# Performance work log

Hardware: AMD Instinct MI355X
Metric: run time of the kernel (lower is better)

The kernel has to match this reference:

```python
import jax, jax.numpy as jnp
import numpy as np

D_MODEL = 384
N_HEAD = 6
HEAD_SIZE = 64
T_LEN = 256
BATCH = 128


def layernorm(x, g, b, eps=1e-5):
    mu = jnp.mean(x, axis=-1, keepdims=True)
    var = jnp.mean(jnp.square(x - mu), axis=-1, keepdims=True)
    return (x - mu) * jax.lax.rsqrt(var + eps) * g + b


def setup_inputs() -> dict:
    key = jax.random.key(0)
    ks = jax.random.split(key, 16)
    s = 0.02
    return {
        "x": jax.random.normal(ks[0], (BATCH, T_LEN, D_MODEL), jnp.float32),
        "Wq": jax.random.normal(ks[1], (N_HEAD, D_MODEL, HEAD_SIZE), jnp.float32) * s,
        "Wk": jax.random.normal(ks[2], (N_HEAD, D_MODEL, HEAD_SIZE), jnp.float32) * s,
        "Wv": jax.random.normal(ks[3], (N_HEAD, D_MODEL, HEAD_SIZE), jnp.float32) * s,
        "Wp": jax.random.normal(ks[4], (N_HEAD * HEAD_SIZE, D_MODEL), jnp.float32) * s,
        "bp": jnp.zeros((D_MODEL,), jnp.float32),
        "W1": jax.random.normal(ks[5], (D_MODEL, 4 * D_MODEL), jnp.float32) * s,
        "b1": jnp.zeros((4 * D_MODEL,), jnp.float32),
        "W2": jax.random.normal(ks[6], (4 * D_MODEL, D_MODEL), jnp.float32) * s,
        "b2": jnp.zeros((D_MODEL,), jnp.float32),
        "g1": jnp.ones((D_MODEL,), jnp.float32),
        "be1": jnp.zeros((D_MODEL,), jnp.float32),
        "g2": jnp.ones((D_MODEL,), jnp.float32),
        "be2": jnp.zeros((D_MODEL,), jnp.float32),
    }


def reference(x, Wq, Wk, Wv, Wp, bp, W1, b1, W2, b2, g1, be1, g2, be2):
    B, T, C = x.shape
    # --- pre-LN causal multi-head attention ---
    h = layernorm(x, g1, be1)
    q = jnp.einsum('btd,hde->bhte', h, Wq)  # [B,H,T,E]
    k = jnp.einsum('btd,hde->bhte', h, Wk)
    v = jnp.einsum('btd,hde->bhte', h, Wv)
    scores = jnp.einsum('bhte,bhse->bhts', q, k) / jnp.sqrt(jnp.float32(HEAD_SIZE))
    causal = jnp.tril(jnp.ones((T, T), bool))
    scores = jnp.where(causal, scores, jnp.float32(-jnp.inf))
    wei = jax.nn.softmax(scores, axis=-1)  # dropout = identity (eval)
    out = jnp.einsum('bhts,bhse->bhte', wei, v)
    out = out.transpose(0, 2, 1, 3).reshape(B, T, N_HEAD * HEAD_SIZE)  # head-concat
    x = x + out @ Wp + bp
    # --- pre-LN FFN ---
    h2 = layernorm(x, g2, be2)
    ff = jax.nn.relu(h2 @ W1 + b1) @ W2 + b2
    return x + ff
```

## Files before the change

kernel.cpp:

```cpp
#include <hip/hip_runtime.h>
#include <hip/hip_bf16.h>

#define D_MODEL 384
#define N_HEAD  6
#define HEAD    64
#define T_LEN   256
#define BATCH   128
#define MROWS   (BATCH * T_LEN)
#define FF      1536

typedef __bf16 bf16x8 __attribute__((ext_vector_type(8)));
typedef float  f32x4  __attribute__((ext_vector_type(4)));
typedef unsigned short us8 __attribute__((ext_vector_type(8)));
typedef unsigned short us4 __attribute__((ext_vector_type(4)));
using bf16 = __hip_bfloat16;

__device__ inline f32x4 mfma16(bf16x8 a, bf16x8 b, f32x4 c) {
    return __builtin_amdgcn_mfma_f32_16x16x32_bf16(a, b, c, 0, 0, 0);
}

#define GLOAD_LDS16(g, l) __builtin_amdgcn_global_load_lds( \
    (const __attribute__((address_space(1))) unsigned int*)(g), \
    (__attribute__((address_space(3))) unsigned int*)(l), 16, 0, 0)

__global__ __launch_bounds__(256) void prep_w(
    const float* __restrict__ Wq, const float* __restrict__ Wk, const float* __restrict__ Wv,
    const float* __restrict__ Wp, const float* __restrict__ W1, const float* __restrict__ W2,
    bf16* __restrict__ Wqkv_t, bf16* __restrict__ Wp_t,
    bf16* __restrict__ W1_t,   bf16* __restrict__ W2_t)
{
    int i = blockIdx.x * 256 + threadIdx.x;
    if (i < 1152 * 384) {
        int cc = i / 384, d = i - cc * 384;
        const float* src = cc < 384 ? Wq : (cc < 768 ? Wk : Wv);
        int c = cc < 384 ? cc : (cc < 768 ? cc - 384 : cc - 768);
        int h = c >> 6, e = c & 63;
        Wqkv_t[i] = __float2bfloat16(src[(h * 384 + d) * 64 + e]);
    }
    if (i < 384 * 384) {
        int o = i / 384, d = i - o * 384;
        Wp_t[i] = __float2bfloat16(Wp[d * 384 + o]);
    }
    if (i < 1536 * 384) {
        int o = i / 384, d = i - o * 384;
        W1_t[i] = __float2bfloat16(W1[d * 1536 + o]);
        int o2 = i / 1536, d2 = i - o2 * 1536;
        W2_t[i] = __float2bfloat16(W2[d2 * 384 + o2]);
    }
}

__global__ __launch_bounds__(256) void ln_k(
    const float* __restrict__ xin, const float* __restrict__ gg,
    const float* __restrict__ bb, bf16* __restrict__ outb)
{
    int wid  = blockIdx.x * 4 + (threadIdx.x >> 6);
    int lane = threadIdx.x & 63;
    const float* xr = xin + (size_t)wid * 384;
    float v[6]; float s = 0.f;
#pragma unroll
    for (int i = 0; i < 6; ++i) { v[i] = xr[lane + i * 64]; s += v[i]; }
#pragma unroll
    for (int mk = 1; mk < 64; mk <<= 1) s += __shfl_xor(s, mk);
    float mu = s * (1.f / 384.f);
    float vs = 0.f;
#pragma unroll
    for (int i = 0; i < 6; ++i) { float d = v[i] - mu; vs += d * d; }
#pragma unroll
    for (int mk = 1; mk < 64; mk <<= 1) vs += __shfl_xor(vs, mk);
    float rs = rsqrtf(vs * (1.f / 384.f) + 1e-5f);
    bf16* orow = outb + (size_t)wid * 384;
#pragma unroll
    for (int i = 0; i < 6; ++i) {
        int c = lane + i * 64;
        orow[c] = __float2bfloat16((v[i] - mu) * rs * gg[c] + bb[c]);
    }
}

__global__ __launch_bounds__(256) void tr_v(
    const bf16* __restrict__ qkv, bf16* __restrict__ vT)
{
    __shared__ bf16 L[256][68];
    int bh = blockIdx.x;
    int b = bh / N_HEAD, h = bh - b * N_HEAD;
    int tid = threadIdx.x;
    const bf16* src = qkv + (size_t)(b * T_LEN + tid) * 1152 + 768 + h * 64;
#pragma unroll
    for (int c = 0; c < 8; ++c)
        *(us8*)&L[tid][c * 8] = *(const us8*)&src[c * 8];
    __syncthreads();
    bf16* dst = vT + (size_t)bh * HEAD * T_LEN;
#pragma unroll
    for (int i = 0; i < 8; ++i) {
        int idx = tid + i * 256;
        int e = idx >> 5, tc = (idx & 31) * 8;
        bf16x8 pk;
#pragma unroll
        for (int j = 0; j < 8; ++j) pk[j] = *(__bf16*)&L[tc + j][e];
        *(bf16x8*)&dst[(size_t)e * T_LEN + tc] = pk;
    }
}

enum { EPI_QKV = 0, EPI_PROJ = 1, EPI_FFN1 = 2, EPI_FFN2 = 3 };

template<int EPI, int K, int NTN>
__global__ __launch_bounds__(256, 2) void gemm8(
    const bf16* __restrict__ A, const bf16* __restrict__ Bt,
    const float* __restrict__ bias, const float* __restrict__ resid,
    float* __restrict__ outf, bf16* __restrict__ outq, bf16* __restrict__ outb)
{
    extern __shared__ char smem[];
    bf16* Albase = (bf16*)smem;
    bf16* Blbase = (bf16*)(smem + 32768);
    constexpr int NT = K / 64;
    constexpr int nwg = (MROWS / 128) * NTN;
    int bid = blockIdx.x;
    int wg = (bid & 7) * (nwg >> 3) + (bid >> 3);
    int mt = wg / NTN, nt = wg - mt * NTN;
    int m0 = mt * 128, n0 = nt * 128;
    int tid = threadIdx.x, lane = tid & 63, w = tid >> 6;
    int r = lane & 15, g = lane >> 4;
    int lr8 = lane >> 3, l7 = lane & 7;
    int csw = (l7 ^ lr8) << 3;
    int wm = (w >> 1) * 64, wn = (w & 1) * 64;
    int sb = g ^ l7;

    const bf16* Ag = A  + (size_t)(m0 + w * 32 + lr8) * K + csw;
    const bf16* Bg = Bt + (size_t)(n0 + w * 32 + lr8) * K + csw;
    const int L0 = w * 2048;

#define STAGE(tt, bb) do { \
    const bf16* a_ = Ag + (tt) * 64; \
    const bf16* b_ = Bg + (tt) * 64; \
    bf16* al_ = Albase + (bb) * 8192 + L0; \
    bf16* bl_ = Blbase + (bb) * 8192 + L0; \
    _Pragma("unroll") for (int q_ = 0; q_ < 4; ++q_) \
        GLOAD_LDS16(a_ + (size_t)q_ * 8 * K, al_ + q_ * 512); \
    _Pragma("unroll") for (int q_ = 0; q_ < 4; ++q_) \
        GLOAD_LDS16(b_ + (size_t)q_ * 8 * K, bl_ + q_ * 512); \
} while (0)

    f32x4 acc[4][4];
#pragma unroll
    for (int i = 0; i < 4; ++i)
#pragma unroll
        for (int j = 0; j < 4; ++j) acc[i][j] = (f32x4){0.f, 0.f, 0.f, 0.f};

    STAGE(0, 0);
    STAGE(1, 1);

#define ITER(tt, VMS, DOSTAGE) do { \
    int bb_ = (tt) & 1; \
    asm volatile("s_waitcnt vmcnt(" VMS ")" ::: "memory"); \
    __builtin_amdgcn_s_barrier(); \
    __builtin_amdgcn_sched_barrier(0); \
    const bf16* Ar_ = Albase + bb_ * 8192; \
    const bf16* Br_ = Blbase + bb_ * 8192; \
    _Pragma("unroll") for (int kk = 0; kk < 2; ++kk) { \
        int so_ = (sb ^ (kk * 4)) << 3; \
        bf16x8 af[4], bfv[4]; \
        _Pragma("unroll") for (int mi = 0; mi < 4; ++mi) \
            af[mi] = *(const bf16x8*)&Ar_[(wm + mi * 16 + r) * 64 + so_]; \
        _Pragma("unroll") for (int ni = 0; ni < 4; ++ni) \
            bfv[ni] = *(const bf16x8*)&Br_[(wn + ni * 16 + r) * 64 + so_]; \
        asm volatile("s_waitcnt lgkmcnt(0)" ::: "memory"); \
        __builtin_amdgcn_sched_barrier(0); \
        __builtin_amdgcn_s_setprio(1); \
        _Pragma("unroll") for (int mi = 0; mi < 4; ++mi) \
            _Pragma("unroll") for (int ni = 0; ni < 4; ++ni) \
                acc[mi][ni] = mfma16(bfv[ni], af[mi], acc[mi][ni]); \
        __builtin_amdgcn_s_setprio(0); \
    } \
    __builtin_amdgcn_s_barrier(); \
    if (DOSTAGE) STAGE((tt) + 2, bb_); \
} while (0)

#pragma unroll 1
    for (int t = 0; t < NT - 2; ++t) ITER(t, "8", true);
    ITER(NT - 2, "8", false);
    ITER(NT - 1, "0", false);
#undef ITER
#undef STAGE

#pragma unroll
    for (int mi = 0; mi < 4; ++mi) {
        size_t m = m0 + wm + mi * 16 + r;
#pragma unroll
        for (int ni = 0; ni < 4; ++ni) {
            int nb = n0 + wn + ni * 16 + (g << 2);
            f32x4 a = acc[mi][ni];
            if constexpr (EPI == EPI_QKV) {
                us4 u;
#pragma unroll
                for (int j = 0; j < 4; ++j) {
                    __bf16 hb = (__bf16)a[j];
                    u[j] = __builtin_bit_cast(unsigned short, hb);
                }
                *(us4*)&outq[m * 1152 + nb] = u;
            } else if constexpr (EPI == EPI_FFN1) {
                f32x4 b4 = *(const f32x4*)&bias[nb];
                us4 u;
#pragma unroll
                for (int j = 0; j < 4; ++j) {
                    float z = a[j] + b4[j]; z = z > 0.f ? z : 0.f;
                    __bf16 hb = (__bf16)z;
                    u[j] = __builtin_bit_cast(unsigned short, hb);
                }
                *(us4*)&outb[m * FF + nb] = u;
            } else {
                f32x4 b4 = *(const f32x4*)&bias[nb];
                f32x4 rv = *(const f32x4*)&resid[m * 384 + nb];
                f32x4 o;
#pragma unroll
                for (int j = 0; j < 4; ++j) o[j] = rv[j] + a[j] + b4[j];
                *(f32x4*)&outf[m * 384 + nb] = o;
            }
        }
    }
}

__global__ __launch_bounds__(256) void attn_k(
    const bf16* __restrict__ qkv, const bf16* __restrict__ vT,
    bf16* __restrict__ att)
{
    __shared__ bf16 Ksm[2][64][64];
    __shared__ bf16 Vsm[2][64][64];
    __shared__ bf16 Psm[4][16][72];
    int bid = blockIdx.x;
    int wg = (bid & 7) * 384 + (bid >> 3);
    int qt = wg & 3, bh = wg >> 2;
    int b = bh / N_HEAD, h = bh - b * N_HEAD;
    int q0 = qt * 64;
    int tid = threadIdx.x, lane = tid & 63, w = tid >> 6;
    int r = lane & 15, g = lane >> 4, ko = g << 3;
    int lr = lane >> 3, l7 = lane & 7;
    int csw = (l7 ^ lr) << 3;
    int r7 = r & 7;

    const bf16* qbase = qkv + (size_t)b * T_LEN * 1152 + h * 64;
    const bf16* kbase = qbase + 384;
    const bf16* vbase = vT + (size_t)bh * HEAD * T_LEN;

#define STAGEA(st, bb) do { \
    int s0_ = (st) * 64; \
    _Pragma("unroll") for (int s_ = 0; s_ < 2; ++s_) { \
        int row0_ = w * 16 + s_ * 8; \
        GLOAD_LDS16(kbase + (size_t)(s0_ + row0_ + lr) * 1152 + csw, &Ksm[bb][row0_][0]); \
        GLOAD_LDS16(vbase + (size_t)(row0_ + lr) * T_LEN + s0_ + csw, &Vsm[bb][row0_][0]); \
    } \
} while (0)

    STAGEA(0, 0);

    bf16x8 qf[2];
    qf[0] = *(const bf16x8*)&qbase[(size_t)(q0 + w * 16 + r) * 1152 + ko];
    qf[1] = *(const bf16x8*)&qbase[(size_t)(q0 + w * 16 + r) * 1152 + ko + 32];

    f32x4 o[4];
#pragma unroll
    for (int i = 0; i < 4; ++i) o[i] = (f32x4){0.f, 0.f, 0.f, 0.f};
    float mrow[4], lrow[4];
#pragma unroll
    for (int j = 0; j < 4; ++j) { mrow[j] = -3.0e38f; lrow[j] = 0.f; }

    for (int st = 0; st <= qt; ++st) {
        int buf = st & 1;
        __syncthreads();
        if (st < qt) STAGEA(st + 1, buf ^ 1);

        f32x4 s[4];
#pragma unroll
        for (int i = 0; i < 4; ++i) s[i] = (f32x4){0.f, 0.f, 0.f, 0.f};
#pragma unroll
        for (int kk = 0; kk < 2; ++kk) {
#pragma unroll
            for (int ni = 0; ni < 4; ++ni) {
                bf16x8 kf = *(const bf16x8*)&Ksm[buf][ni * 16 + r][((4 * kk + g) ^ r7) << 3];
                s[ni] = mfma16(qf[kk], kf, s[ni]);
            }
        }
        int qrow = q0 + w * 16 + (g << 2);
        int s0 = st * 64;
        float tmax[4], fsc[4], tsum[4];
#pragma unroll
        for (int j = 0; j < 4; ++j) {
            float mx = -3.0e38f;
#pragma unroll
            for (int ni = 0; ni < 4; ++ni) {
                int col = s0 + ni * 16 + r;
                float sv = (col <= qrow + j) ? s[ni][j] * 0.125f : -3.0e38f;
                s[ni][j] = sv;
                mx = fmaxf(mx, sv);
            }
            tmax[j] = mx;
        }
#pragma unroll
        for (int mk = 1; mk < 16; mk <<= 1)
#pragma unroll
            for (int j = 0; j < 4; ++j) tmax[j] = fmaxf(tmax[j], __shfl_xor(tmax[j], mk));
#pragma unroll
        for (int j = 0; j < 4; ++j) {
            float mnew = fmaxf(mrow[j], tmax[j]);
            fsc[j] = __expf(mrow[j] - mnew);
            mrow[j] = mnew;
            float ss = 0.f;
#pragma unroll
            for (int ni = 0; ni < 4; ++ni) {
                float p = __expf(s[ni][j] - mnew);
                s[ni][j] = p; ss += p;
            }
            tsum[j] = ss;
        }
#pragma unroll
        for (int mk = 1; mk < 16; mk <<= 1)
#pragma unroll
            for (int j = 0; j < 4; ++j) tsum[j] += __shfl_xor(tsum[j], mk);
#pragma unroll
        for (int j = 0; j < 4; ++j) lrow[j] = lrow[j] * fsc[j] + tsum[j];
#pragma unroll
        for (int ni = 0; ni < 4; ++ni)
#pragma unroll
            for (int j = 0; j < 4; ++j) o[ni][j] *= fsc[j];
#pragma unroll
        for (int ni = 0; ni < 4; ++ni)
#pragma unroll
            for (int j = 0; j < 4; ++j)
                Psm[w][(g << 2) + j][ni * 16 + r] = __float2bfloat16(s[ni][j]);
#pragma unroll
        for (int kk = 0; kk < 2; ++kk) {
            bf16x8 pf = *(const bf16x8*)&Psm[w][r][kk * 32 + ko];
#pragma unroll
            for (int ni = 0; ni < 4; ++ni) {
                bf16x8 vf = *(const bf16x8*)&Vsm[buf][ni * 16 + r][((4 * kk + g) ^ r7) << 3];
                o[ni] = mfma16(pf, vf, o[ni]);
            }
        }
    }
#undef STAGEA

#pragma unroll
    for (int ni = 0; ni < 4; ++ni)
#pragma unroll
        for (int j = 0; j < 4; ++j) {
            int t = q0 + w * 16 + (g << 2) + j;
            int e = h * HEAD + ni * 16 + r;
            att[((size_t)b * T_LEN + t) * D_MODEL + e] = __float2bfloat16(o[ni][j] / lrow[j]);
        }
}

#define GEMM_SMEM 65536

extern "C" void kernel_launch(void* const* d_in, const int* in_sizes, int n_in,
                              void* d_out, int out_size, void* d_ws, size_t ws_size,
                              hipStream_t stream)
{
    const float* x   = (const float*)d_in[0];
    const float* Wq  = (const float*)d_in[1];
    const float* Wk  = (const float*)d_in[2];
    const float* Wv  = (const float*)d_in[3];
    const float* Wp  = (const float*)d_in[4];
    const float* bp  = (const float*)d_in[5];
    const float* W1  = (const float*)d_in[6];
    const float* b1  = (const float*)d_in[7];
    const float* W2  = (const float*)d_in[8];
    const float* b2  = (const float*)d_in[9];
    const float* g1  = (const float*)d_in[10];
    const float* be1 = (const float*)d_in[11];
    const float* g2  = (const float*)d_in[12];
    const float* be2 = (const float*)d_in[13];
    float* out = (float*)d_out;

    char* ws = (char*)d_ws;
    size_t off = 0;
    auto alloc = [&](size_t bytes) { void* p = ws + off; off += (bytes + 255) & ~(size_t)255; return p; };
    bf16* Wqkv_t = (bf16*)alloc((size_t)1152 * 384 * 2);
    bf16* Wp_t   = (bf16*)alloc((size_t)384 * 384 * 2);
    bf16* W1_t   = (bf16*)alloc((size_t)1536 * 384 * 2);
    bf16* W2_t   = (bf16*)alloc((size_t)384 * 1536 * 2);
    bf16* h      = (bf16*)alloc((size_t)MROWS * 384 * 2);
    bf16* qkv    = (bf16*)alloc((size_t)MROWS * 1152 * 2);
    bf16* attb   = (bf16*)alloc((size_t)MROWS * 384 * 2);
    float* x1    = (float*)alloc((size_t)MROWS * 384 * 4);
    bf16* vTb    = h;
    bf16* ff1    = qkv;

    hipFuncSetAttribute(reinterpret_cast<const void*>(&gemm8<EPI_QKV, 384, 9>),
                        hipFuncAttributeMaxDynamicSharedMemorySize, GEMM_SMEM);
    hipFuncSetAttribute(reinterpret_cast<const void*>(&gemm8<EPI_PROJ, 384, 3>),
                        hipFuncAttributeMaxDynamicSharedMemorySize, GEMM_SMEM);
    hipFuncSetAttribute(reinterpret_cast<const void*>(&gemm8<EPI_FFN1, 384, 12>),
                        hipFuncAttributeMaxDynamicSharedMemorySize, GEMM_SMEM);
    hipFuncSetAttribute(reinterpret_cast<const void*>(&gemm8<EPI_FFN2, 1536, 3>),
                        hipFuncAttributeMaxDynamicSharedMemorySize, GEMM_SMEM);

    prep_w<<<2304, 256, 0, stream>>>(Wq, Wk, Wv, Wp, W1, W2, Wqkv_t, Wp_t, W1_t, W2_t);
    ln_k<<<MROWS / 4, 256, 0, stream>>>(x, g1, be1, h);
    gemm8<EPI_QKV, 384, 9><<<2304, 256, GEMM_SMEM, stream>>>(
        h, Wqkv_t, nullptr, nullptr, nullptr, qkv, nullptr);
    tr_v<<<BATCH * N_HEAD, 256, 0, stream>>>(qkv, vTb);
    attn_k<<<BATCH * N_HEAD * 4, 256, 0, stream>>>(qkv, vTb, attb);
    gemm8<EPI_PROJ, 384, 3><<<768, 256, GEMM_SMEM, stream>>>(
        attb, Wp_t, bp, x, x1, nullptr, nullptr);
    ln_k<<<MROWS / 4, 256, 0, stream>>>(x1, g2, be2, h);
    gemm8<EPI_FFN1, 384, 12><<<3072, 256, GEMM_SMEM, stream>>>(
        h, W1_t, b1, nullptr, nullptr, nullptr, ff1);
    gemm8<EPI_FFN2, 1536, 3><<<768, 256, GEMM_SMEM, stream>>>(
        ff1, W2_t, b2, x1, out, nullptr, nullptr);
}
```

Before: 302.1 us.

## Drop GEMM double buffering for single-buffered static LDS at higher occupancy

Replaces the hand-scheduled double-buffered GEMM mainloop (explicit vmcnt waits, sched barriers, setprio) with a simple single-buffered loop using static 32KB shared memory and two __syncthreads per K tile. Launch bounds rise from 2 to 4 blocks per CU, relying on extra waves to hide global-to-LDS latency instead of software prefetch. The exchange is lost intra-block overlap between loads and MFMA, plus extra barriers, for potentially more concurrent blocks, with register pressure possibly constrained by the tighter bound.

```diff
diff --git a/kernel.cpp b/kernel.cpp
--- a/kernel.cpp
+++ b/kernel.cpp
@@ -103,14 +103,13 @@
 enum { EPI_QKV = 0, EPI_PROJ = 1, EPI_FFN1 = 2, EPI_FFN2 = 3 };
 
 template<int EPI, int K, int NTN>
-__global__ __launch_bounds__(256, 2) void gemm8(
+__global__ __launch_bounds__(256, 4) void gemm8(
     const bf16* __restrict__ A, const bf16* __restrict__ Bt,
     const float* __restrict__ bias, const float* __restrict__ resid,
     float* __restrict__ outf, bf16* __restrict__ outq, bf16* __restrict__ outb)
 {
-    extern __shared__ char smem[];
-    bf16* Albase = (bf16*)smem;
-    bf16* Blbase = (bf16*)(smem + 32768);
+    __shared__ bf16 Asm[128][64];
+    __shared__ bf16 Bsm[128][64];
     constexpr int NT = K / 64;
     constexpr int nwg = (MROWS / 128) * NTN;
     int bid = blockIdx.x;
@@ -126,18 +125,8 @@
 
     const bf16* Ag = A  + (size_t)(m0 + w * 32 + lr8) * K + csw;
     const bf16* Bg = Bt + (size_t)(n0 + w * 32 + lr8) * K + csw;
-    const int L0 = w * 2048;
-
-#define STAGE(tt, bb) do { \
-    const bf16* a_ = Ag + (tt) * 64; \
-    const bf16* b_ = Bg + (tt) * 64; \
-    bf16* al_ = Albase + (bb) * 8192 + L0; \
-    bf16* bl_ = Blbase + (bb) * 8192 + L0; \
-    _Pragma("unroll") for (int q_ = 0; q_ < 4; ++q_) \
-        GLOAD_LDS16(a_ + (size_t)q_ * 8 * K, al_ + q_ * 512); \
-    _Pragma("unroll") for (int q_ = 0; q_ < 4; ++q_) \
-        GLOAD_LDS16(b_ + (size_t)q_ * 8 * K, bl_ + q_ * 512); \
-} while (0)
+    bf16* Al = &Asm[w * 32][0];
+    bf16* Bl = &Bsm[w * 32][0];
 
     f32x4 acc[4][4];
 #pragma unroll
@@ -145,41 +134,34 @@
 #pragma unroll
         for (int j = 0; j < 4; ++j) acc[i][j] = (f32x4){0.f, 0.f, 0.f, 0.f};
 
-    STAGE(0, 0);
-    STAGE(1, 1);
-
-#define ITER(tt, VMS, DOSTAGE) do { \
-    int bb_ = (tt) & 1; \
-    asm volatile("s_waitcnt vmcnt(" VMS ")" ::: "memory"); \
-    __builtin_amdgcn_s_barrier(); \
-    __builtin_amdgcn_sched_barrier(0); \
-    const bf16* Ar_ = Albase + bb_ * 8192; \
-    const bf16* Br_ = Blbase + bb_ * 8192; \
-    _Pragma("unroll") for (int kk = 0; kk < 2; ++kk) { \
-        int so_ = (sb ^ (kk * 4)) << 3; \
-        bf16x8 af[4], bfv[4]; \
-        _Pragma("unroll") for (int mi = 0; mi < 4; ++mi) \
-            af[mi] = *(const bf16x8*)&Ar_[(wm + mi * 16 + r) * 64 + so_]; \
-        _Pragma("unroll") for (int ni = 0; ni < 4; ++ni) \
-            bfv[ni] = *(const bf16x8*)&Br_[(wn + ni * 16 + r) * 64 + so_]; \
-        asm volatile("s_waitcnt lgkmcnt(0)" ::: "memory"); \
-        __builtin_amdgcn_sched_barrier(0); \
-        __builtin_amdgcn_s_setprio(1); \
-        _Pragma("unroll") for (int mi = 0; mi < 4; ++mi) \
-            _Pragma("unroll") for (int ni = 0; ni < 4; ++ni) \
-                acc[mi][ni] = mfma16(bfv[ni], af[mi], acc[mi][ni]); \
-        __builtin_amdgcn_s_setprio(0); \
-    } \
-    __builtin_amdgcn_s_barrier(); \
-    if (DOSTAGE) STAGE((tt) + 2, bb_); \
-} while (0)
-
 #pragma unroll 1
-    for (int t = 0; t < NT - 2; ++t) ITER(t, "8", true);
-    ITER(NT - 2, "8", false);
-    ITER(NT - 1, "0", false);
-#undef ITER
-#undef STAGE
+    for (int t = 0; t < NT; ++t) {
+        const bf16* a_ = Ag + t * 64;
+        const bf16* b_ = Bg + t * 64;
+#pragma unroll
+        for (int q = 0; q < 4; ++q) {
+            GLOAD_LDS16(a_ + (size_t)q * 8 * K, Al + q * 512);
+            GLOAD_LDS16(b_ + (size_t)q * 8 * K, Bl + q * 512);
+        }
+        __syncthreads();
+#pragma unroll
+        for (int kk = 0; kk < 2; ++kk) {
+            int so = (sb ^ (kk * 4)) << 3;
+            bf16x8 af[4], bfv[4];
+#pragma unroll
+            for (int mi = 0; mi < 4; ++mi)
+                af[mi] = *(const bf16x8*)&Asm[wm + mi * 16 + r][so];
+#pragma unroll
+            for (int ni = 0; ni < 4; ++ni)
+                bfv[ni] = *(const bf16x8*)&Bsm[wn + ni * 16 + r][so];
+#pragma unroll
+            for (int mi = 0; mi < 4; ++mi)
+#pragma unroll
+                for (int ni = 0; ni < 4; ++ni)
+                    acc[mi][ni] = mfma16(bfv[ni], af[mi], acc[mi][ni]);
+        }
+        __syncthreads();
+    }
 
 #pragma unroll
     for (int mi = 0; mi < 4; ++mi) {
@@ -346,8 +328,6 @@
             att[((size_t)b * T_LEN + t) * D_MODEL + e] = __float2bfloat16(o[ni][j] / lrow[j]);
         }
 }
-
-#define GEMM_SMEM 65536
 
 extern "C" void kernel_launch(void* const* d_in, const int* in_sizes, int n_in,
                               void* d_out, int out_size, void* d_ws, size_t ws_size,
@@ -383,26 +363,17 @@
     bf16* vTb    = h;
     bf16* ff1    = qkv;
 
-    hipFuncSetAttribute(reinterpret_cast<const void*>(&gemm8<EPI_QKV, 384, 9>),
-                        hipFuncAttributeMaxDynamicSharedMemorySize, GEMM_SMEM);
-    hipFuncSetAttribute(reinterpret_cast<const void*>(&gemm8<EPI_PROJ, 384, 3>),
-                        hipFuncAttributeMaxDynamicSharedMemorySize, GEMM_SMEM);
-    hipFuncSetAttribute(reinterpret_cast<const void*>(&gemm8<EPI_FFN1, 384, 12>),
-                        hipFuncAttributeMaxDynamicSharedMemorySize, GEMM_SMEM);
-    hipFuncSetAttribute(reinterpret_cast<const void*>(&gemm8<EPI_FFN2, 1536, 3>),
-                        hipFuncAttributeMaxDynamicSharedMemorySize, GEMM_SMEM);
-
     prep_w<<<2304, 256, 0, stream>>>(Wq, Wk, Wv, Wp, W1, W2, Wqkv_t, Wp_t, W1_t, W2_t);
     ln_k<<<MROWS / 4, 256, 0, stream>>>(x, g1, be1, h);
-    gemm8<EPI_QKV, 384, 9><<<2304, 256, GEMM_SMEM, stream>>>(
+    gemm8<EPI_QKV, 384, 9><<<2304, 256, 0, stream>>>(
         h, Wqkv_t, nullptr, nullptr, nullptr, qkv, nullptr);
     tr_v<<<BATCH * N_HEAD, 256, 0, stream>>>(qkv, vTb);
     attn_k<<<BATCH * N_HEAD * 4, 256, 0, stream>>>(qkv, vTb, attb);
-    gemm8<EPI_PROJ, 384, 3><<<768, 256, GEMM_SMEM, stream>>>(
+    gemm8<EPI_PROJ, 384, 3><<<768, 256, 0, stream>>>(
         attb, Wp_t, bp, x, x1, nullptr, nullptr);
     ln_k<<<MROWS / 4, 256, 0, stream>>>(x1, g2, be2, h);
-    gemm8<EPI_FFN1, 384, 12><<<3072, 256, GEMM_SMEM, stream>>>(
+    gemm8<EPI_FFN1, 384, 12><<<3072, 256, 0, stream>>>(
         h, W1_t, b1, nullptr, nullptr, nullptr, ff1);
-    gemm8<EPI_FFN2, 1536, 3><<<768, 256, GEMM_SMEM, stream>>>(
+    gemm8<EPI_FFN2, 1536, 3><<<768, 256, 0, stream>>>(
         ff1, W2_t, b2, x1, out, nullptr, nullptr);
 }
```

Measured after the change: 297.4 us. Within noise of the previous version (-1.6%).
